# Performance work log

Measured on AMD Instinct MI355X. Metric: run time of the kernel, lower is better.

Reference implementation:

```python
import jax, jax.numpy as jnp
import numpy as np


def _chamfer(pred, tgt):
    # pred: [B,N,3], tgt: [B,M,3]
    # Euclidean pairwise distances (same math as torch.cdist, p=2)
    p2 = jnp.sum(pred * pred, axis=-1)              # [B,N]
    t2 = jnp.sum(tgt * tgt, axis=-1)                # [B,M]
    cross = jnp.einsum('bnd,bmd->bnm', pred, tgt)   # [B,N,M]
    sq = p2[:, :, None] + t2[:, None, :] - 2.0 * cross
    dist = jnp.sqrt(jnp.maximum(sq, 0.0))           # [B,N,M]
    min_p2t = jnp.min(dist, axis=2)                 # [B,N]
    min_t2p = jnp.min(dist, axis=1)                 # [B,M]
    return jnp.mean(min_p2t) + jnp.mean(min_t2p)


def setup_inputs() -> dict:
    key = jax.random.key(0)
    k1, k2 = jax.random.split(key)
    B, N, M, D = 8, 4096, 4096, 3
    predicted_points = jax.random.normal(k1, (B, N, D), dtype=jnp.float32)
    target_points = jax.random.normal(k2, (B, M, D), dtype=jnp.float32)
    return {"predicted_points": predicted_points, "target_points": target_points}


def reference(predicted_points, target_points):
    return _chamfer(predicted_points, target_points)
```

## Files before the change

### kernel.cpp

```cpp
#include <hip/hip_runtime.h>
#include <math.h>

#define B_SZ 8
#define N_SZ 4096
#define M_SZ 4096
#define NQ (B_SZ * N_SZ)
#define TOT (2 * NQ)

#define THREADS 256
#define QPT 16
#define QPB (THREADS * QPT)
#define JTILE 128
#define NJT (M_SZ / JTILE)

#define NBLK2 (TOT / 256)

typedef float f32x2 __attribute__((ext_vector_type(2)));

__global__ __launch_bounds__(THREADS)
void chamfer_partial_kernel(const float* __restrict__ pred,
                            const float* __restrict__ tgt,
                            float* __restrict__ part)
{
    const int b   = blockIdx.y;
    const int dir = blockIdx.z;

    const float* Q;
    const float* Db;
    int qoff;
    if (dir == 0) { Q = pred + (size_t)b * N_SZ * 3; Db = tgt  + (size_t)b * M_SZ * 3; qoff = b * N_SZ; }
    else          { Q = tgt  + (size_t)b * M_SZ * 3; Db = pred + (size_t)b * N_SZ * 3; qoff = NQ + b * M_SZ; }

    const int g = blockIdx.x;

    __shared__ float sA[JTILE * 2];
    __shared__ float sB[JTILE * 2];
    if (threadIdx.x < JTILE) {
        const float* s = Db + (size_t)(g * JTILE + threadIdx.x) * 3;
        float x = s[0], y = s[1], z = s[2];
        float h = 0.5f * (x * x + y * y + z * z);
        const int p = threadIdx.x >> 1, l = threadIdx.x & 1;
        sA[4 * p + l]     = x;
        sA[4 * p + 2 + l] = y;
        sB[4 * p + l]     = z;
        sB[4 * p + 2 + l] = h;
    }
    __syncthreads();

    f32x2 qxs[QPT], qys[QPT], qzs[QPT];
    float mn[QPT], q2h[QPT];
#pragma unroll
    for (int k = 0; k < QPT; ++k) {
        const int i = threadIdx.x + k * THREADS;
        float x = Q[i * 3 + 0], y = Q[i * 3 + 1], z = Q[i * 3 + 2];
        qxs[k] = { -x, -x };
        qys[k] = { -y, -y };
        qzs[k] = { -z, -z };
        q2h[k] = 0.5f * (x * x + y * y + z * z);
        mn[k]  = 3.0e38f;
    }

    const float4* A4 = (const float4*)sA;
    const float4* B4 = (const float4*)sB;

#pragma unroll 2
    for (int jp = 0; jp < JTILE / 2; ++jp) {
        float4 A = A4[jp];
        float4 B = B4[jp];
        f32x2 tx = { A.x, A.y };
        f32x2 ty = { A.z, A.w };
        f32x2 tz = { B.x, B.y };
        f32x2 th = { B.z, B.w };
#pragma unroll
        for (int k = 0; k < QPT; ++k) {
            f32x2 sc = th + qxs[k] * tx;
            sc += qys[k] * ty;
            sc += qzs[k] * tz;
            mn[k] = fminf(fminf(mn[k], sc.x), sc.y);
        }
    }

    float* pg = part + (size_t)g * TOT + qoff;
#pragma unroll
    for (int k = 0; k < QPT; ++k) {
        pg[threadIdx.x + k * THREADS] = mn[k] + q2h[k];
    }
}

__global__ __launch_bounds__(256)
void chamfer_combine_kernel(const float* __restrict__ part,
                            float* __restrict__ bsum)
{
    const int q = blockIdx.x * 256 + threadIdx.x;
    float m = 3.0e38f;
#pragma unroll
    for (int g = 0; g < NJT; ++g) m = fminf(m, part[(size_t)g * TOT + q]);
    float d = sqrtf(2.0f * fmaxf(m, 0.0f));
#pragma unroll
    for (int off = 32; off > 0; off >>= 1) d += __shfl_down(d, off);
    __shared__ float r[4];
    if ((threadIdx.x & 63) == 0) r[threadIdx.x >> 6] = d;
    __syncthreads();
    if (threadIdx.x == 0) bsum[blockIdx.x] = r[0] + r[1] + r[2] + r[3];
}

__global__ __launch_bounds__(64)
void chamfer_final_kernel(const float* __restrict__ bsum,
                          float* __restrict__ out)
{
    float s = 0.0f;
#pragma unroll
    for (int i = 0; i < NBLK2 / 64; ++i) s += bsum[threadIdx.x + i * 64];
#pragma unroll
    for (int off = 32; off > 0; off >>= 1) s += __shfl_down(s, off);
    if (threadIdx.x == 0) out[0] = s * (1.0f / (float)NQ);
}

extern "C" void kernel_launch(void* const* d_in, const int* in_sizes, int n_in,
                              void* d_out, int out_size, void* d_ws, size_t ws_size,
                              hipStream_t stream) {
    const float* pred = (const float*)d_in[0];
    const float* tgt  = (const float*)d_in[1];
    float* out = (float*)d_out;

    float* part = (float*)d_ws;
    float* bsum = part + (size_t)NJT * TOT;

    dim3 grid1(NJT, B_SZ, 2);
    chamfer_partial_kernel<<<grid1, THREADS, 0, stream>>>(pred, tgt, part);
    chamfer_combine_kernel<<<NBLK2, 256, 0, stream>>>(part, bsum);
    chamfer_final_kernel<<<1, 64, 0, stream>>>(bsum, out);
}
```

Before: 81.24 us.

## Pre-pack target tiles in global memory and read them directly instead of LDS

Adds a pack kernel that writes each cloud's points as interleaved float4 pairs (x,y / z,half-norm) into workspace. The partial kernel then drops its shared-memory staging and __syncthreads and loads the packed pairs straight from global memory, which are uniform across the block and can go through the scalar/constant cache path. It also switches to explicit packed FMAs and raises the unroll factor. The cost is an extra kernel launch and a global write/read of the packed array, and the inner loop now depends on global-load latency rather than LDS.

```diff
diff --git a/kernel.cpp b/kernel.cpp
--- a/kernel.cpp
+++ b/kernel.cpp
@@ -9,46 +9,55 @@
 
 #define THREADS 256
 #define QPT 16
-#define QPB (THREADS * QPT)
 #define JTILE 128
 #define NJT (M_SZ / JTILE)
-
+#define PAIRS_PER_CLOUD (M_SZ / 2)
 #define NBLK2 (TOT / 256)
 
 typedef float f32x2 __attribute__((ext_vector_type(2)));
 
+
+__global__ __launch_bounds__(256)
+void chamfer_pack_kernel(const float* __restrict__ pred,
+                         const float* __restrict__ tgt,
+                         float4* __restrict__ TT)
+{
+    const int pid = blockIdx.x * 256 + threadIdx.x;
+    const int lp  = pid & (PAIRS_PER_CLOUD - 1);
+    const int cb  = pid >> 11;
+    const int dir = cb >> 3;
+    const int b   = cb & (B_SZ - 1);
+    const float* Db = (dir == 0) ? (tgt  + (size_t)b * M_SZ * 3)
+                                 : (pred + (size_t)b * N_SZ * 3);
+    const float* s = Db + (size_t)(2 * lp) * 3;
+    float x0 = s[0], y0 = s[1], z0 = s[2];
+    float x1 = s[3], y1 = s[4], z1 = s[5];
+    float h0 = 0.5f * (x0 * x0 + y0 * y0 + z0 * z0);
+    float h1 = 0.5f * (x1 * x1 + y1 * y1 + z1 * z1);
+    TT[2 * pid]     = make_float4(x0, x1, y0, y1);
+    TT[2 * pid + 1] = make_float4(z0, z1, h0, h1);
+}
+
 __global__ __launch_bounds__(THREADS)
 void chamfer_partial_kernel(const float* __restrict__ pred,
                             const float* __restrict__ tgt,
+                            const float4* __restrict__ TT,
                             float* __restrict__ part)
 {
     const int b   = blockIdx.y;
     const int dir = blockIdx.z;
+    const int g   = blockIdx.x;
 
     const float* Q;
-    const float* Db;
     int qoff;
-    if (dir == 0) { Q = pred + (size_t)b * N_SZ * 3; Db = tgt  + (size_t)b * M_SZ * 3; qoff = b * N_SZ; }
-    else          { Q = tgt  + (size_t)b * M_SZ * 3; Db = pred + (size_t)b * N_SZ * 3; qoff = NQ + b * M_SZ; }
+    if (dir == 0) { Q = pred + (size_t)b * N_SZ * 3; qoff = b * N_SZ; }
+    else          { Q = tgt  + (size_t)b * M_SZ * 3; qoff = NQ + b * M_SZ; }
 
-    const int g = blockIdx.x;
-
-    __shared__ float sA[JTILE * 2];
-    __shared__ float sB[JTILE * 2];
-    if (threadIdx.x < JTILE) {
-        const float* s = Db + (size_t)(g * JTILE + threadIdx.x) * 3;
-        float x = s[0], y = s[1], z = s[2];
-        float h = 0.5f * (x * x + y * y + z * z);
-        const int p = threadIdx.x >> 1, l = threadIdx.x & 1;
-        sA[4 * p + l]     = x;
-        sA[4 * p + 2 + l] = y;
-        sB[4 * p + l]     = z;
-        sB[4 * p + 2 + l] = h;
-    }
-    __syncthreads();
+    const float4* __restrict__ S =
+        TT + (size_t)((dir * B_SZ + b) * PAIRS_PER_CLOUD + g * (JTILE / 2)) * 2;
 
     f32x2 qxs[QPT], qys[QPT], qzs[QPT];
-    float mn[QPT], q2h[QPT];
+    float q2h[QPT], mn[QPT];
 #pragma unroll
     for (int k = 0; k < QPT; ++k) {
         const int i = threadIdx.x + k * THREADS;
@@ -60,23 +69,20 @@
         mn[k]  = 3.0e38f;
     }
 
-    const float4* A4 = (const float4*)sA;
-    const float4* B4 = (const float4*)sB;
-
-#pragma unroll 2
+#pragma unroll 4
     for (int jp = 0; jp < JTILE / 2; ++jp) {
-        float4 A = A4[jp];
-        float4 B = B4[jp];
-        f32x2 tx = { A.x, A.y };
-        f32x2 ty = { A.z, A.w };
-        f32x2 tz = { B.x, B.y };
-        f32x2 th = { B.z, B.w };
+        const float4 A  = S[2 * jp];
+        const float4 Bv = S[2 * jp + 1];
+        const f32x2 txx = { A.x,  A.y  };
+        const f32x2 tyy = { A.z,  A.w  };
+        const f32x2 tzz = { Bv.x, Bv.y };
+        const f32x2 thh = { Bv.z, Bv.w };
 #pragma unroll
         for (int k = 0; k < QPT; ++k) {
-            f32x2 sc = th + qxs[k] * tx;
-            sc += qys[k] * ty;
-            sc += qzs[k] * tz;
-            mn[k] = fminf(fminf(mn[k], sc.x), sc.y);
+            f32x2 sc = __builtin_elementwise_fma(qzs[k], tzz, thh);
+            sc       = __builtin_elementwise_fma(qys[k], tyy, sc);
+            sc       = __builtin_elementwise_fma(qxs[k], txx, sc);
+            mn[k] = fminf(mn[k], fminf(sc.x, sc.y));
         }
     }
 
@@ -123,11 +129,15 @@
     const float* tgt  = (const float*)d_in[1];
     float* out = (float*)d_out;
 
-    float* part = (float*)d_ws;
-    float* bsum = part + (size_t)NJT * TOT;
+    float*  part = (float*)d_ws;
+    float*  bsum = part + (size_t)NJT * TOT;
+    float4* TT   = (float4*)(bsum + NBLK2);
+
+    chamfer_pack_kernel<<<(2 * B_SZ * PAIRS_PER_CLOUD) / 256, 256, 0, stream>>>(
+        pred, tgt, TT);
 
     dim3 grid1(NJT, B_SZ, 2);
-    chamfer_partial_kernel<<<grid1, THREADS, 0, stream>>>(pred, tgt, part);
+    chamfer_partial_kernel<<<grid1, THREADS, 0, stream>>>(pred, tgt, TT, part);
     chamfer_combine_kernel<<<NBLK2, 256, 0, stream>>>(part, bsum);
     chamfer_final_kernel<<<1, 64, 0, stream>>>(bsum, out);
 }
```

Result: slower. 86.14 us (+6.0%).
